# Kernel optimization log

Hardware: AMD Instinct MI355X
Metric: run time of the kernel (lower is better)

## Reference

```python
import jax, jax.numpy as jnp
import numpy as np

B, SQ, SK, D, H, DH = 4, 1024, 1024, 1024, 16, 64

def setup_inputs() -> dict:
    key = jax.random.key(0)
    ks = jax.random.split(key, 7)
    s = 0.02
    return {
        "input_ids": jax.random.normal(ks[0], (B, SQ, D), jnp.float32),
        "encoder_output": jax.random.normal(ks[1], (B, SK, D), jnp.float32),
        "position_bias": jax.random.normal(ks[2], (1, H, SQ, SK), jnp.float32),
        "Wq": jax.random.normal(ks[3], (D, H * DH), jnp.float32) * s,
        "Wk": jax.random.normal(ks[4], (D, H * DH), jnp.float32) * s,
        "Wv": jax.random.normal(ks[5], (D, H * DH), jnp.float32) * s,
        "Wo": jax.random.normal(ks[6], (H * DH, D), jnp.float32) * s,
    }

def reference(input_ids, encoder_output, position_bias, Wq, Wk, Wv, Wo):
    # bias-free projections (nn.Linear(..., bias=False))
    q = (input_ids @ Wq).reshape(B, SQ, H, DH).transpose(0, 2, 1, 3)      # [B,H,Sq,dh]
    k = (encoder_output @ Wk).reshape(B, SK, H, DH).transpose(0, 2, 1, 3)  # [B,H,Sk,dh]
    v = (encoder_output @ Wv).reshape(B, SK, H, DH).transpose(0, 2, 1, 3)  # [B,H,Sk,dh]
    # T5-style attention: NO 1/sqrt(dh) scaling, additive position bias
    scores = jnp.einsum("bhqd,bhkd->bhqk", q, k) + position_bias          # [B,H,Sq,Sk]
    attn = jax.nn.softmax(scores, axis=-1)
    ctx = jnp.einsum("bhqk,bhkd->bhqd", attn, v)                          # [B,H,Sq,dh]
    ctx = ctx.transpose(0, 2, 1, 3).reshape(B, SQ, H * DH)
    return ctx @ Wo                                                        # [B,Sq,D]
```

## Files before the change

kernel.cpp:

```cpp
#include <hip/hip_runtime.h>

typedef _Float16 f16;
typedef _Float16 f16x4 __attribute__((ext_vector_type(4)));
typedef _Float16 f16x8 __attribute__((ext_vector_type(8)));
typedef float f32x4 __attribute__((ext_vector_type(4)));
typedef float f32x16 __attribute__((ext_vector_type(16)));

#define LOADLDS16(gp, lp)                                                     \
  __builtin_amdgcn_global_load_lds(                                           \
      (const __attribute__((address_space(1))) void*)(gp),                    \
      (__attribute__((address_space(3))) void*)(lp), 16, 0, 0)

__global__ __launch_bounds__(256) void k_prep(
    const float* __restrict__ xa, const float* __restrict__ xb,
    f16* __restrict__ ya, f16* __restrict__ yb, const float* __restrict__ w0,
    const float* __restrict__ w1, const float* __restrict__ w2,
    const float* __restrict__ w3, f16* __restrict__ o0, f16* __restrict__ o1,
    f16* __restrict__ o2, f16* __restrict__ o3) {
  __shared__ f16 T[64][72];
  const int tid = threadIdx.x;
  const int bid = blockIdx.x;
  if (bid < 8192) {
    int i = bid * 256 + tid;
    const float* x;
    f16* y;
    if (i < 1048576) {
      x = xa; y = ya;
    } else {
      x = xb; y = yb; i -= 1048576;
    }
    float4 v = reinterpret_cast<const float4*>(x)[i];
    f16x4 o;
    o[0] = (f16)v.x; o[1] = (f16)v.y; o[2] = (f16)v.z; o[3] = (f16)v.w;
    reinterpret_cast<f16x4*>(y)[i] = o;
    return;
  }
  const int bid2 = bid - 8192;
  const int z = bid2 >> 8, yb_ = (bid2 >> 4) & 15, xb_ = bid2 & 15;
  const float* W;
  f16* O;
  switch (z) {
    case 0: W = w0; O = o0; break;
    case 1: W = w1; O = o1; break;
    case 2: W = w2; O = o2; break;
    default: W = w3; O = o3; break;
  }
  const int r0 = yb_ * 64, c0 = xb_ * 64;
#pragma unroll
  for (int i = 0; i < 4; ++i) {
    int c = i * 256 + tid;
    int row = c >> 4, col = (c & 15) * 4;
    float4 v = *reinterpret_cast<const float4*>(W + (size_t)(r0 + row) * 1024 + c0 + col);
    T[col + 0][row] = (f16)v.x;
    T[col + 1][row] = (f16)v.y;
    T[col + 2][row] = (f16)v.z;
    T[col + 3][row] = (f16)v.w;
  }
  __syncthreads();
#pragma unroll
  for (int i = 0; i < 2; ++i) {
    int c = i * 256 + tid;
    int cc = c >> 3, ro = (c & 7) * 8;
    f16x8 v;
#pragma unroll
    for (int j = 0; j < 8; ++j) v[j] = T[cc][ro + j];
    *reinterpret_cast<f16x8*>(O + (size_t)(c0 + cc) * 1024 + r0 + ro) = v;
  }
}

__global__ __launch_bounds__(256) void k_gemm_qkv(const f16* __restrict__ Xq,
                                                  const f16* __restrict__ Xkv,
                                                  const f16* __restrict__ Bt,
                                                  f16* __restrict__ outp) {
  __shared__ f16 As[128 * 64];
  __shared__ f16 Bs[128 * 64];
  const int tid = threadIdx.x;
  const int w = tid >> 6, l = tid & 63;
  const int lr = l & 15, lq = l >> 4;
  const int flat = blockIdx.y * 24 + blockIdx.x;
  const int ord = (flat & 7) * 96 + (flat >> 3);
  const int m0 = (ord / 24) * 128, n0 = (ord % 24) * 128;
  const f16* A = (n0 < 1024) ? Xq : Xkv;
  const int wr = (w >> 1) * 64, wc = (w & 1) * 64;
  const int K = 1024;
  const bool vplane = (n0 >= 2048);
  f32x4 acc[4][4] = {};
  for (int kt = 0; kt < K; kt += 64) {
#pragma unroll
    for (int i = 0; i < 4; ++i) {
      int c = (i * 4 + w) * 64 + l;
      LOADLDS16(A + (size_t)(m0 + (c >> 3)) * K + kt + (c & 7) * 8,
                As + (size_t)(i * 4 + w) * 512);
      LOADLDS16(Bt + (size_t)(n0 + (c >> 3)) * K + kt + (c & 7) * 8,
                Bs + (size_t)(i * 4 + w) * 512);
    }
    __syncthreads();
#pragma unroll
    for (int kk = 0; kk < 2; ++kk) {
      f16x8 af[4], bf[4];
#pragma unroll
      for (int m = 0; m < 4; ++m)
        af[m] = *reinterpret_cast<const f16x8*>(As + (wr + m * 16 + lr) * 64 + kk * 32 + lq * 8);
#pragma unroll
      for (int n = 0; n < 4; ++n)
        bf[n] = *reinterpret_cast<const f16x8*>(Bs + (wc + n * 16 + lr) * 64 + kk * 32 + lq * 8);
      if (vplane) {
#pragma unroll
        for (int m = 0; m < 4; ++m)
#pragma unroll
          for (int n = 0; n < 4; ++n)
            acc[m][n] = __builtin_amdgcn_mfma_f32_16x16x32_f16(af[m], bf[n], acc[m][n], 0, 0, 0);
      } else {
#pragma unroll
        for (int m = 0; m < 4; ++m)
#pragma unroll
          for (int n = 0; n < 4; ++n)
            acc[m][n] = __builtin_amdgcn_mfma_f32_16x16x32_f16(bf[n], af[m], acc[m][n], 0, 0, 0);
      }
    }
    __syncthreads();
  }
  if (vplane) {
#pragma unroll
    for (int m = 0; m < 4; ++m)
#pragma unroll
      for (int n = 0; n < 4; ++n) {
        int col = n0 + wc + n * 16 + lr;
        int row0 = m0 + wr + m * 16 + lq * 4;
        int b = row0 >> 10, s0 = row0 & 1023;
        int cc = col & 1023;
        int h = cc >> 6, dh = cc & 63;
        f16x4 v4;
#pragma unroll
        for (int r = 0; r < 4; ++r) v4[r] = (f16)acc[m][n][r];
        *reinterpret_cast<f16x4*>(
            outp + (size_t)2 * 4194304 +
            ((size_t)(b * 16 + h)) * 65536 + (size_t)dh * 1024 + s0) = v4;
      }
  } else {
#pragma unroll
    for (int m = 0; m < 4; ++m)
#pragma unroll
      for (int n = 0; n < 4; ++n) {
        int row0 = m0 + wr + m * 16 + lr;
        int col0 = n0 + wc + n * 16 + lq * 4;
        int b = row0 >> 10, sidx = row0 & 1023;
        int plane = col0 >> 10, cc = col0 & 1023;
        int h = cc >> 6, dh0 = cc & 63;
        f16x4 v4;
#pragma unroll
        for (int r = 0; r < 4; ++r) v4[r] = (f16)acc[m][n][r];
        *reinterpret_cast<f16x4*>(
            outp + (size_t)plane * 4194304 +
            (((size_t)(b * 16 + h)) * 1024 + sidx) * 64 + dh0) = v4;
      }
  }
}

__global__ __launch_bounds__(256) void k_gemm_o(const f16* __restrict__ A,
                                                const f16* __restrict__ Bt,
                                                float* __restrict__ out, int M,
                                                int N, int K) {
  __shared__ f16 As[64 * 64];
  __shared__ f16 Bs[128 * 64];
  const int tid = threadIdx.x;
  const int w = tid >> 6, l = tid & 63;
  const int lr = l & 15, lq = l >> 4;
  const int flat = blockIdx.y * 8 + blockIdx.x;
  const int ord = (flat & 7) * 64 + (flat >> 3);
  const int m0 = (ord >> 3) * 64, n0 = (ord & 7) * 128;
  const int wr = (w >> 1) * 32, wc = (w & 1) * 64;
  f32x4 acc[2][4] = {};
  for (int kt = 0; kt < K; kt += 64) {
#pragma unroll
    for (int i = 0; i < 2; ++i) {
      int c = (i * 4 + w) * 64 + l;
      LOADLDS16(A + (size_t)(m0 + (c >> 3)) * K + kt + (c & 7) * 8,
                As + (size_t)(i * 4 + w) * 512);
    }
#pragma unroll
    for (int i = 0; i < 4; ++i) {
      int c = (i * 4 + w) * 64 + l;
      LOADLDS16(Bt + (size_t)(n0 + (c >> 3)) * K + kt + (c & 7) * 8,
                Bs + (size_t)(i * 4 + w) * 512);
    }
    __syncthreads();
#pragma unroll
    for (int kk = 0; kk < 2; ++kk) {
      f16x8 af[2], bf[4];
#pragma unroll
      for (int m = 0; m < 2; ++m)
        af[m] = *reinterpret_cast<const f16x8*>(As + (wr + m * 16 + lr) * 64 + kk * 32 + lq * 8);
#pragma unroll
      for (int n = 0; n < 4; ++n)
        bf[n] = *reinterpret_cast<const f16x8*>(Bs + (wc + n * 16 + lr) * 64 + kk * 32 + lq * 8);
#pragma unroll
      for (int m = 0; m < 2; ++m)
#pragma unroll
        for (int n = 0; n < 4; ++n)
          acc[m][n] = __builtin_amdgcn_mfma_f32_16x16x32_f16(af[m], bf[n], acc[m][n], 0, 0, 0);
    }
    __syncthreads();
  }
#pragma unroll
  for (int m = 0; m < 2; ++m)
#pragma unroll
    for (int n = 0; n < 4; ++n)
#pragma unroll
      for (int r = 0; r < 4; ++r) {
        int row = m0 + wr + m * 16 + lq * 4 + r;
        int col = n0 + wc + n * 16 + lr;
        out[(size_t)row * N + col] = acc[m][n][r];
      }
}

__global__ __launch_bounds__(256, 2) void k_attn(const f16* __restrict__ qb,
                                                 const f16* __restrict__ kb,
                                                 const f16* __restrict__ vtb,
                                                 const float* __restrict__ bias,
                                                 f16* __restrict__ ctx) {
  const int bid = blockIdx.x;
  const int ord = (bid & 7) * 64 + (bid >> 3);
  const int h = ord >> 5, b = (ord >> 3) & 3, qt = ord & 7;
  const int bh = b * 16 + h;
  const int q0 = qt * 128;
  const int tid = threadIdx.x, w = tid >> 6, l = tid & 63;
  const int l31 = l & 31, xi = l >> 5;
  const int qw = q0 + w * 32;

  __shared__ f16 Kb[2][4096];
  __shared__ f16 Vb[2][4096];

  const f16* qp = qb + ((size_t)bh * 1024 + qw + l31) * 64 + xi * 8;
  f16x8 qf[4];
#pragma unroll
  for (int s = 0; s < 4; ++s)
    qf[s] = *reinterpret_cast<const f16x8*>(qp + s * 16);

  f32x16 O[2] = {};
  float mrun = -3.0e38f, rsum = 0.f;

  const f16* kbase = kb + (size_t)bh * 65536;
  const f16* vbase = vtb + (size_t)bh * 65536;
  const float* bq =
      bias + ((size_t)h * 1024 + qw + l31) * 1024 + 4 * xi;

  auto stage = [&](int t, int nxt) {
#pragma unroll
    for (int i = 0; i < 2; ++i) {
      int c = (i * 4 + w) * 64 + l;
      int row = c >> 3, g = (c & 7) ^ (row & 7);
      LOADLDS16(kbase + (size_t)(t * 64 + row) * 64 + g * 8,
                &Kb[nxt][(i * 4 + w) * 512]);
      LOADLDS16(vbase + (size_t)row * 1024 + t * 64 + g * 8,
                &Vb[nxt][(i * 4 + w) * 512]);
    }
  };

  stage(0, 0);

#pragma unroll 1
  for (int t = 0; t < 16; ++t) {
    const int cur = t & 1;
    __builtin_amdgcn_s_barrier();
    f32x4 bf[2][4];
#pragma unroll
    for (int c = 0; c < 2; ++c)
#pragma unroll
      for (int g = 0; g < 4; ++g)
        bf[c][g] = *reinterpret_cast<const f32x4*>(bq + t * 64 + c * 32 + 8 * g);
    __builtin_amdgcn_sched_barrier(0);
    if (t < 15) stage(t + 1, cur ^ 1);
    __builtin_amdgcn_sched_barrier(0);
    if (t < 15) {
      asm volatile("s_waitcnt vmcnt(12)" ::: "memory");
    } else {
      asm volatile("s_waitcnt vmcnt(8)" ::: "memory");
    }
    __builtin_amdgcn_sched_barrier(0);

    f32x16 S[2];
#pragma unroll
    for (int c = 0; c < 2; ++c) {
#pragma unroll
      for (int g = 0; g < 4; ++g)
#pragma unroll
        for (int e = 0; e < 4; ++e) S[c][4 * g + e] = bf[c][g][e];
    }
    __builtin_amdgcn_s_setprio(1);
#pragma unroll
    for (int c = 0; c < 2; ++c) {
      int row = c * 32 + l31, s7 = l31 & 7;
      const f16* kbp = &Kb[cur][row * 64];
#pragma unroll
      for (int s = 0; s < 4; ++s) {
        f16x8 kf = *reinterpret_cast<const f16x8*>(kbp + (((2 * s + xi) ^ s7) * 8));
        S[c] = __builtin_amdgcn_mfma_f32_32x32x16_f16(kf, qf[s], S[c], 0, 0, 0);
      }
    }
    __builtin_amdgcn_s_setprio(0);

    float tmax = -3.0e38f;
#pragma unroll
    for (int c = 0; c < 2; ++c)
#pragma unroll
      for (int r = 0; r < 16; ++r) tmax = fmaxf(tmax, S[c][r]);
    if (!__all(tmax <= mrun + 8.0f)) {
      tmax = fmaxf(tmax, __shfl_xor(tmax, 32, 64));
      float mnew = fmaxf(mrun, tmax);
      float sc = __expf(mrun - mnew);
      mrun = mnew;
      rsum *= sc;
#pragma unroll
      for (int d = 0; d < 2; ++d)
#pragma unroll
        for (int r = 0; r < 16; ++r) O[d][r] *= sc;
    }

    f16x4 qd[2][4];
#pragma unroll
    for (int c = 0; c < 2; ++c)
#pragma unroll
      for (int g = 0; g < 4; ++g) {
        f32x4 p;
#pragma unroll
        for (int e = 0; e < 4; ++e) p[e] = __expf(S[c][4 * g + e] - mrun);
        rsum += (p[0] + p[1]) + (p[2] + p[3]);
        f16x4 ph = {(f16)p[0], (f16)p[1], (f16)p[2], (f16)p[3]};
        qd[c][g] = ph;
      }

    f16x8 pb[4];
#pragma unroll
    for (int c = 0; c < 2; ++c)
#pragma unroll
      for (int v = 0; v < 2; ++v) {
        union { f16x4 h; unsigned int u[2]; } snd, rcv;
        snd.h = xi ? qd[c][2 * v] : qd[c][2 * v + 1];
        rcv.u[0] = __shfl_xor(snd.u[0], 32, 64);
        rcv.u[1] = __shfl_xor(snd.u[1], 32, 64);
        f16x4 own = xi ? qd[c][2 * v + 1] : qd[c][2 * v];
        f16x4 q1 = xi ? rcv.h : own;
        f16x4 q2 = xi ? own : rcv.h;
        f16x8 t8;
#pragma unroll
        for (int j = 0; j < 4; ++j) {
          t8[j] = q1[j];
          t8[4 + j] = q2[j];
        }
        pb[2 * c + v] = t8;
      }

    __builtin_amdgcn_s_setprio(1);
#pragma unroll
    for (int d = 0; d < 2; ++d) {
      int row = d * 32 + l31, s7 = l31 & 7;
      const f16* vbp = &Vb[cur][row * 64];
#pragma unroll
      for (int u = 0; u < 4; ++u) {
        f16x8 vf = *reinterpret_cast<const f16x8*>(vbp + (((2 * u + xi) ^ s7) * 8));
        O[d] = __builtin_amdgcn_mfma_f32_32x32x16_f16(vf, pb[u], O[d], 0, 0, 0);
      }
    }
    __builtin_amdgcn_s_setprio(0);
    __builtin_amdgcn_sched_barrier(0);
  }

  rsum += __shfl_xor(rsum, 32, 64);
  float inv = 1.0f / rsum;

  const int q = qw + l31;
  f16* cp = ctx + ((size_t)b * 1024 + q) * 1024 + h * 64;
#pragma unroll
  for (int d = 0; d < 2; ++d)
#pragma unroll
    for (int g = 0; g < 4; ++g) {
      f16x4 v4;
#pragma unroll
      for (int e = 0; e < 4; ++e) v4[e] = (f16)(O[d][4 * g + e] * inv);
      *reinterpret_cast<f16x4*>(cp + d * 32 + 8 * g + 4 * xi) = v4;
    }
}

extern "C" void kernel_launch(void* const* d_in, const int* in_sizes, int n_in,
                              void* d_out, int out_size, void* d_ws,
                              size_t ws_size, hipStream_t stream) {
  const float* input_ids = (const float*)d_in[0];
  const float* enc = (const float*)d_in[1];
  const float* bias = (const float*)d_in[2];
  const float* Wq = (const float*)d_in[3];
  const float* Wk = (const float*)d_in[4];
  const float* Wv = (const float*)d_in[5];
  const float* Wo = (const float*)d_in[6];

  char* ws = (char*)d_ws;
  const size_t MB = 1024 * 1024;
  f16* Xq  = (f16*)(ws + 0 * MB);
  f16* Xkv = (f16*)(ws + 8 * MB);
  f16* Wqt = (f16*)(ws + 16 * MB);
  f16* Wkt = (f16*)(ws + 18 * MB);
  f16* Wvt = (f16*)(ws + 20 * MB);
  f16* Wot = (f16*)(ws + 22 * MB);
  f16* qbuf = (f16*)(ws + 24 * MB);
  f16* kbuf = (f16*)(ws + 32 * MB);
  f16* vtb  = (f16*)(ws + 40 * MB);
  f16* ctxb = Xq;

  k_prep<<<9216, 256, 0, stream>>>(input_ids, enc, Xq, Xkv, Wq, Wk, Wv, Wo,
                                   Wqt, Wkt, Wvt, Wot);

  k_gemm_qkv<<<dim3(24, 32), 256, 0, stream>>>(Xq, Xkv, Wqt, qbuf);

  k_attn<<<512, 256, 0, stream>>>(qbuf, kbuf, vtb, bias, ctxb);

  k_gemm_o<<<dim3(8, 64), 256, 0, stream>>>(ctxb, Wot, (float*)d_out, 4096, 1024, 1024);
}
```

Before: 136.8 us.

## Split attention KV range in two with a log-sum-exp combine kernel

Adds a split-KV mode to the attention kernel. Each (batch, head, q-tile) block is split into two blocks, each covering half of the key range, giving 1024 blocks instead of 512. Each half writes a normalized partial context and its log-sum-exp, and a new combine kernel merges the two halves into the context buffer. Workspace is reshuffled to hold the partials, and the mode is enabled only when the workspace is large enough. The intent is more parallelism per query tile, at the cost of extra partial-result traffic, a second launch and a duplicated Q-load prologue.

```diff
diff --git a/kernel.cpp b/kernel.cpp
--- a/kernel.cpp
+++ b/kernel.cpp
@@ -214,14 +214,22 @@
       }
 }
 
-__global__ __launch_bounds__(256, 2) void k_attn(const f16* __restrict__ qb,
-                                                 const f16* __restrict__ kb,
-                                                 const f16* __restrict__ vtb,
-                                                 const float* __restrict__ bias,
-                                                 f16* __restrict__ ctx) {
+__global__ __launch_bounds__(256, 2) void k_attn(
+    const f16* __restrict__ qb, const f16* __restrict__ kb,
+    const f16* __restrict__ vtb, const float* __restrict__ bias,
+    f16* __restrict__ ctx, f16* __restrict__ opart, float* __restrict__ lsebuf,
+    int split) {
   const int bid = blockIdx.x;
-  const int ord = (bid & 7) * 64 + (bid >> 3);
-  const int h = ord >> 5, b = (ord >> 3) & 3, qt = ord & 7;
+  int h, b, qt, kvh;
+  if (split) {
+    const int ord = (bid & 7) * 128 + (bid >> 3);
+    h = ord >> 6; b = (ord >> 4) & 3; qt = (ord >> 1) & 7; kvh = ord & 1;
+  } else {
+    const int ord = (bid & 7) * 64 + (bid >> 3);
+    h = ord >> 5; b = (ord >> 3) & 3; qt = ord & 7; kvh = 0;
+  }
+  const int nt = split ? 8 : 16;
+  const int kvoff = kvh * 8;
   const int bh = b * 16 + h;
   const int q0 = qt * 128;
   const int tid = threadIdx.x, w = tid >> 6, l = tid & 63;
@@ -242,25 +250,24 @@
 
   const f16* kbase = kb + (size_t)bh * 65536;
   const f16* vbase = vtb + (size_t)bh * 65536;
-  const float* bq =
-      bias + ((size_t)h * 1024 + qw + l31) * 1024 + 4 * xi;
-
-  auto stage = [&](int t, int nxt) {
+  const float* bq = bias + ((size_t)h * 1024 + qw + l31) * 1024 + 4 * xi;
+
+  auto stage = [&](int gt, int nxt) {
 #pragma unroll
     for (int i = 0; i < 2; ++i) {
       int c = (i * 4 + w) * 64 + l;
       int row = c >> 3, g = (c & 7) ^ (row & 7);
-      LOADLDS16(kbase + (size_t)(t * 64 + row) * 64 + g * 8,
+      LOADLDS16(kbase + (size_t)(gt * 64 + row) * 64 + g * 8,
                 &Kb[nxt][(i * 4 + w) * 512]);
-      LOADLDS16(vbase + (size_t)row * 1024 + t * 64 + g * 8,
+      LOADLDS16(vbase + (size_t)row * 1024 + gt * 64 + g * 8,
                 &Vb[nxt][(i * 4 + w) * 512]);
     }
   };
 
-  stage(0, 0);
+  stage(kvoff, 0);
 
 #pragma unroll 1
-  for (int t = 0; t < 16; ++t) {
+  for (int t = 0; t < nt; ++t) {
     const int cur = t & 1;
     __builtin_amdgcn_s_barrier();
     f32x4 bf[2][4];
@@ -268,11 +275,12 @@
     for (int c = 0; c < 2; ++c)
 #pragma unroll
       for (int g = 0; g < 4; ++g)
-        bf[c][g] = *reinterpret_cast<const f32x4*>(bq + t * 64 + c * 32 + 8 * g);
+        bf[c][g] = *reinterpret_cast<const f32x4*>(
+            bq + (kvoff + t) * 64 + c * 32 + 8 * g);
     __builtin_amdgcn_sched_barrier(0);
-    if (t < 15) stage(t + 1, cur ^ 1);
+    if (t < nt - 1) stage(kvoff + t + 1, cur ^ 1);
     __builtin_amdgcn_sched_barrier(0);
-    if (t < 15) {
+    if (t < nt - 1) {
       asm volatile("s_waitcnt vmcnt(12)" ::: "memory");
     } else {
       asm volatile("s_waitcnt vmcnt(8)" ::: "memory");
@@ -368,18 +376,53 @@
 
   rsum += __shfl_xor(rsum, 32, 64);
   float inv = 1.0f / rsum;
-
   const int q = qw + l31;
-  f16* cp = ctx + ((size_t)b * 1024 + q) * 1024 + h * 64;
-#pragma unroll
-  for (int d = 0; d < 2; ++d)
-#pragma unroll
-    for (int g = 0; g < 4; ++g) {
-      f16x4 v4;
-#pragma unroll
-      for (int e = 0; e < 4; ++e) v4[e] = (f16)(O[d][4 * g + e] * inv);
-      *reinterpret_cast<f16x4*>(cp + d * 32 + 8 * g + 4 * xi) = v4;
-    }
+
+  if (!split) {
+    f16* cp = ctx + ((size_t)b * 1024 + q) * 1024 + h * 64;
+#pragma unroll
+    for (int d = 0; d < 2; ++d)
+#pragma unroll
+      for (int g = 0; g < 4; ++g) {
+        f16x4 v4;
+#pragma unroll
+        for (int e = 0; e < 4; ++e) v4[e] = (f16)(O[d][4 * g + e] * inv);
+        *reinterpret_cast<f16x4*>(cp + d * 32 + 8 * g + 4 * xi) = v4;
+      }
+  } else {
+    f16* op = opart + (size_t)kvh * 4194304 + ((size_t)bh * 1024 + q) * 64;
+#pragma unroll
+    for (int d = 0; d < 2; ++d)
+#pragma unroll
+      for (int g = 0; g < 4; ++g) {
+        f16x4 v4;
+#pragma unroll
+        for (int e = 0; e < 4; ++e) v4[e] = (f16)(O[d][4 * g + e] * inv);
+        *reinterpret_cast<f16x4*>(op + d * 32 + 8 * g + 4 * xi) = v4;
+      }
+    if (xi == 0)
+      lsebuf[((size_t)kvh * 64 + bh) * 1024 + q] = mrun + __logf(rsum);
+  }
+}
+
+__global__ __launch_bounds__(256) void k_combine(const f16* __restrict__ opart,
+                                                 const float* __restrict__ lsebuf,
+                                                 f16* __restrict__ ctx) {
+  int idx = blockIdx.x * 256 + threadIdx.x;
+  int g8 = idx & 7, row = idx >> 3;
+  int bh = row >> 10, q = row & 1023;
+  float l0 = lsebuf[row], l1 = lsebuf[65536 + row];
+  float L = fmaxf(l0, l1);
+  float w0 = __expf(l0 - L), w1 = __expf(l1 - L);
+  float inv = 1.0f / (w0 + w1);
+  f16x8 a = *reinterpret_cast<const f16x8*>(opart + (size_t)row * 64 + g8 * 8);
+  f16x8 c = *reinterpret_cast<const f16x8*>(opart + 4194304 + (size_t)row * 64 + g8 * 8);
+  f16x8 o;
+#pragma unroll
+  for (int j = 0; j < 8; ++j)
+    o[j] = (f16)((w0 * (float)a[j] + w1 * (float)c[j]) * inv);
+  int b = bh >> 4, h = bh & 15;
+  *reinterpret_cast<f16x8*>(ctx + ((size_t)b * 1024 + q) * 1024 + h * 64 + g8 * 8) = o;
 }
 
 extern "C" void kernel_launch(void* const* d_in, const int* in_sizes, int n_in,
@@ -395,15 +438,18 @@
 
   char* ws = (char*)d_ws;
   const size_t MB = 1024 * 1024;
+  const bool split = ws_size >= 51 * MB;
   f16* Xq  = (f16*)(ws + 0 * MB);
   f16* Xkv = (f16*)(ws + 8 * MB);
   f16* Wqt = (f16*)(ws + 16 * MB);
   f16* Wkt = (f16*)(ws + 18 * MB);
   f16* Wvt = (f16*)(ws + 20 * MB);
-  f16* Wot = (f16*)(ws + 22 * MB);
+  f16* Wot = (f16*)(ws + (split ? 48 * MB : 22 * MB));
   f16* qbuf = (f16*)(ws + 24 * MB);
   f16* kbuf = (f16*)(ws + 32 * MB);
   f16* vtb  = (f16*)(ws + 40 * MB);
+  f16* opart = (f16*)(ws + 8 * MB);
+  float* lsebuf = (float*)(ws + 50 * MB);
   f16* ctxb = Xq;
 
   k_prep<<<9216, 256, 0, stream>>>(input_ids, enc, Xq, Xkv, Wq, Wk, Wv, Wo,
@@ -411,7 +457,14 @@
 
   k_gemm_qkv<<<dim3(24, 32), 256, 0, stream>>>(Xq, Xkv, Wqt, qbuf);
 
-  k_attn<<<512, 256, 0, stream>>>(qbuf, kbuf, vtb, bias, ctxb);
+  if (split) {
+    k_attn<<<1024, 256, 0, stream>>>(qbuf, kbuf, vtb, bias, ctxb, opart,
+                                     lsebuf, 1);
+    k_combine<<<2048, 256, 0, stream>>>(opart, lsebuf, ctxb);
+  } else {
+    k_attn<<<512, 256, 0, stream>>>(qbuf, kbuf, vtb, bias, ctxb, opart,
+                                    lsebuf, 0);
+  }
 
   k_gemm_o<<<dim3(8, 64), 256, 0, stream>>>(ctxb, Wot, (float*)d_out, 4096, 1024, 1024);
 }
```

Result: slower. 148.4 us (+8.5%).
